# Optimization experiments

Hardware: AMD Instinct MI355X
Metric: run time of the kernel (lower is better)

The kernel has to match this reference:

```python
import jax, jax.numpy as jnp
import numpy as np

N = 50000
E = 600000
D = 128
HEADS = 4
G = 64  # num graphs
EPS = 1e-5


def setup_inputs() -> dict:
    key = jax.random.key(0)
    ks = jax.random.split(key, 16)
    s = 0.05
    inp = {
        'x': jax.random.normal(ks[0], (N, D), jnp.float32),
        'edge_index': jax.random.randint(ks[1], (2, E), 0, N, jnp.int64),
        'batch': jnp.sort(jax.random.randint(ks[2], (N,), 0, G, jnp.int64)),
        # GCN layer 1
        'W1': jax.random.normal(ks[3], (D, D), jnp.float32) * s,
        'b1': jnp.zeros((D,), jnp.float32),
        'g1': jnp.ones((D,), jnp.float32),
        'beta1': jnp.zeros((D,), jnp.float32),
        # GCN layer 2
        'W2': jax.random.normal(ks[4], (D, D), jnp.float32) * s,
        'b2': jnp.zeros((D,), jnp.float32),
        'g2': jnp.ones((D,), jnp.float32),
        'beta2': jnp.zeros((D,), jnp.float32),
        # GAT (heads=4, concat=False -> mean over heads)
        'gat_W': jax.random.normal(ks[5], (D, HEADS * D), jnp.float32) * s,
        'att_src': jax.random.normal(ks[6], (HEADS, D), jnp.float32) * s,
        'att_dst': jax.random.normal(ks[7], (HEADS, D), jnp.float32) * s,
        'gat_b': jnp.zeros((D,), jnp.float32),
    }
    return inp


def _layer_norm(x, g, b):
    mu = jnp.mean(x, axis=-1, keepdims=True)
    var = jnp.mean((x - mu) ** 2, axis=-1, keepdims=True)
    return (x - mu) * jax.lax.rsqrt(var + EPS) * g + b


def _gcn(x, W, b, src, dst, deg_inv_sqrt):
    h = x @ W                                    # [N, D]
    norm = deg_inv_sqrt[src] * deg_inv_sqrt[dst]  # [E']
    msg = norm[:, None] * h[src]                 # [E', D] gather
    return jax.ops.segment_sum(msg, dst, num_segments=N) + b


def _gat(x, W, b, att_src, att_dst, src, dst):
    h = (x @ W).reshape(N, HEADS, D)             # [N, H, D]
    a_s = jnp.einsum('nhd,hd->nh', h, att_src)   # [N, H]
    a_d = jnp.einsum('nhd,hd->nh', h, att_dst)
    e = jax.nn.leaky_relu(a_s[src] + a_d[dst], 0.2)          # [E', H]
    m = jax.ops.segment_max(e, dst, num_segments=N)          # segment softmax
    ex = jnp.exp(e - m[dst])
    den = jax.ops.segment_sum(ex, dst, num_segments=N)
    alpha = ex / den[dst]                                     # [E', H]
    out = jax.ops.segment_sum(alpha[:, :, None] * h[src], dst, num_segments=N)
    return jnp.mean(out, axis=1) + b             # concat=False -> head mean


def reference(x, edge_index, batch, W1, b1, g1, beta1, W2, b2, g2, beta2,
              gat_W, gat_b, att_src, att_dst):
    # add self loops (PyG default for GCNConv and GATConv)
    loops = jnp.arange(N, dtype=edge_index.dtype)
    src = jnp.concatenate([edge_index[0], loops])
    dst = jnp.concatenate([edge_index[1], loops])
    deg = jax.ops.segment_sum(jnp.ones_like(dst, jnp.float32), dst, num_segments=N)
    deg_inv_sqrt = jnp.where(deg > 0, jax.lax.rsqrt(jnp.maximum(deg, 1.0)), 0.0)

    # GCN stack: conv -> LayerNorm -> relu -> dropout(eval=identity)
    h = jax.nn.relu(_layer_norm(_gcn(x, W1, b1, src, dst, deg_inv_sqrt), g1, beta1))
    h = jax.nn.relu(_layer_norm(_gcn(h, W2, b2, src, dst, deg_inv_sqrt), g2, beta2))

    h = jax.nn.relu(_gat(h, gat_W, gat_b, att_src, att_dst, src, dst))
    node_embeddings = h

    cnt = jax.ops.segment_sum(jnp.ones((N,), jnp.float32), batch, num_segments=G)
    mean_pool = jax.ops.segment_sum(h, batch, num_segments=G) / jnp.maximum(cnt, 1.0)[:, None]
    max_pool = jax.ops.segment_max(h, batch, num_segments=G)
    graph_embedding = jnp.concatenate([mean_pool, max_pool], axis=1)  # [G, 2D]
    return graph_embedding, node_embeddings
```

## Files before the change

### kernel.cpp

```cpp
#include <hip/hip_runtime.h>
#include <math.h>


#define TPB 256

typedef __attribute__((ext_vector_type(8))) short short8;
typedef __attribute__((ext_vector_type(4))) float f32x4;
union U4S8 { uint4 u; short8 s; };

__device__ __forceinline__ float lrelu(float x) { return x > 0.f ? x : 0.2f * x; }

__device__ __forceinline__ unsigned short f2bf(float f) {
    unsigned int u = __float_as_uint(f);
    u += 0x7fffu + ((u >> 16) & 1u);
    return (unsigned short)(u >> 16);
}
__device__ __forceinline__ float2 bf2x(unsigned int u) {
    return make_float2(__uint_as_float(u << 16), __uint_as_float(u & 0xffff0000u));
}
__device__ __forceinline__ float sel4(float4 v, int h) {
    float r = v.x;
    r = (h == 1) ? v.y : r;
    r = (h == 2) ? v.z : r;
    r = (h == 3) ? v.w : r;
    return r;
}
__device__ __forceinline__ float dot4(f32x4 a, float4 b) {
    return a.x * b.x + a.y * b.y + a.z * b.z + a.w * b.w;
}

__global__ __launch_bounds__(TPB) void k_hist(const int* __restrict__ dst,
                                              int* __restrict__ deg, int e) {
    int i = blockIdx.x * TPB + threadIdx.x;
    if (i < e) atomicAdd(&deg[dst[i]], 1);
}

__global__ __launch_bounds__(TPB) void k_scan_part_wt(const int* __restrict__ deg,
                                                      int* __restrict__ part, int n, int nb,
                                                      const float* __restrict__ W1,
                                                      const float* __restrict__ W2,
                                                      const float* __restrict__ Wg,
                                                      unsigned short* __restrict__ Wt1,
                                                      unsigned short* __restrict__ Wt2,
                                                      unsigned short* __restrict__ Wtg) {
    int bid = blockIdx.x;
    if (bid < nb) {
        int i = bid * TPB + threadIdx.x;
        int v = (i < n) ? deg[i] : 0;
#pragma unroll
        for (int o = 32; o > 0; o >>= 1) v += __shfl_xor(v, o);
        __shared__ int sw[4];
        if ((threadIdx.x & 63) == 0) sw[threadIdx.x >> 6] = v;
        __syncthreads();
        if (threadIdx.x == 0) part[bid] = sw[0] + sw[1] + sw[2] + sw[3];
    } else {
        int i = (bid - nb) * TPB + threadIdx.x;
        if (i < 16384) {
            int k = i >> 7, c = i & 127;
            Wt1[c * 128 + k] = f2bf(W1[i]);
        } else if (i < 32768) {
            int j = i - 16384;
            int k = j >> 7, c = j & 127;
            Wt2[c * 128 + k] = f2bf(W2[j]);
        } else if (i < 98304) {
            int j = i - 32768;
            int k = j >> 9, c = j & 511;
            Wtg[c * 128 + k] = f2bf(Wg[j]);
        }
    }
}

__global__ __launch_bounds__(TPB) void k_scan_apply(const int* __restrict__ deg,
                                                    const int* __restrict__ part,
                                                    int* __restrict__ row_start,
                                                    int* __restrict__ cursor,
                                                    float* __restrict__ dis,
                                                    int n, int e_total) {
    __shared__ int sm[TPB];
    __shared__ int sred[4];
    int t = threadIdx.x;
    int bid = blockIdx.x;
    int pv = (t < bid) ? part[t] : 0;
#pragma unroll
    for (int o = 32; o > 0; o >>= 1) pv += __shfl_xor(pv, o);
    if ((t & 63) == 0) sred[t >> 6] = pv;
    __syncthreads();
    int basep = sred[0] + sred[1] + sred[2] + sred[3];
    int i = bid * TPB + t;
    int d = (i < n) ? deg[i] : 0;
    sm[t] = d;
    __syncthreads();
    for (int off = 1; off < TPB; off <<= 1) {
        int u = (t >= off) ? sm[t - off] : 0;
        __syncthreads();
        sm[t] += u;
        __syncthreads();
    }
    if (i < n) {
        int rs = basep + sm[t] - d;
        row_start[i] = rs;
        cursor[i] = rs;
        dis[i] = rsqrtf((float)(d + 1));
    }
    if (bid == 0 && t == 0) row_start[n] = e_total;
}

__global__ __launch_bounds__(TPB, 2) void k_gemm1_scatter(const float* __restrict__ feat,
                                                          const unsigned short* __restrict__ Wt,
                                                          unsigned short* __restrict__ C,
                                                          int nrows, int gb,
                                                          const int* __restrict__ src,
                                                          const int* __restrict__ dst,
                                                          const float* __restrict__ dis,
                                                          int* __restrict__ cursor,
                                                          int* __restrict__ csr_src,
                                                          float* __restrict__ csr_w, int e) {
    __shared__ uint4 wl[2048];
    int t = threadIdx.x;
    if (blockIdx.x >= gb) {
        int i = (blockIdx.x - gb) * TPB + t;
        if (i < e) {
            int s = src[i];
            int p = atomicAdd(&cursor[dst[i]], 1);
            csr_src[p] = s;
            csr_w[p] = dis[s];
        }
        return;
    }
#pragma unroll
    for (int i = 0; i < 8; ++i) {
        int fi = i * 256 + t;
        int l = fi & 63, ct = (fi >> 6) & 7, ks = fi >> 9;
        int chan = ct * 16 + (l & 15);
        wl[fi] = ((const uint4*)(Wt + (size_t)chan * 128))[ks * 4 + (l >> 4)];
    }
    __syncthreads();

    int wave = t >> 6, lane = t & 63;
    int wr = wave >> 1, wc = wave & 1;
    int nbase = (blockIdx.x << 7) + (wc << 6);
    const float4* brow[4];
#pragma unroll
    for (int nt = 0; nt < 4; ++nt) {
        int node = nbase + nt * 16 + (lane & 15);
        node = node < nrows ? node : (nrows - 1);
        brow[nt] = (const float4*)(feat + (size_t)node * 128);
    }
    f32x4 acc[4][4];
#pragma unroll
    for (int mt = 0; mt < 4; ++mt)
#pragma unroll
        for (int nt = 0; nt < 4; ++nt) acc[mt][nt] = (f32x4)0.f;

    int kq = lane >> 4;
#pragma unroll
    for (int ks = 0; ks < 4; ++ks) {
        U4S8 a[4], b[4];
#pragma unroll
        for (int mt = 0; mt < 4; ++mt)
            a[mt].u = wl[(ks * 8 + wr * 4 + mt) * 64 + lane];
#pragma unroll
        for (int nt = 0; nt < 4; ++nt) {
            float4 f0 = brow[nt][ks * 8 + kq * 2];
            float4 f1 = brow[nt][ks * 8 + kq * 2 + 1];
            b[nt].u.x = (unsigned int)f2bf(f0.x) | ((unsigned int)f2bf(f0.y) << 16);
            b[nt].u.y = (unsigned int)f2bf(f0.z) | ((unsigned int)f2bf(f0.w) << 16);
            b[nt].u.z = (unsigned int)f2bf(f1.x) | ((unsigned int)f2bf(f1.y) << 16);
            b[nt].u.w = (unsigned int)f2bf(f1.z) | ((unsigned int)f2bf(f1.w) << 16);
        }
#pragma unroll
        for (int mt = 0; mt < 4; ++mt)
#pragma unroll
            for (int nt = 0; nt < 4; ++nt)
                acc[mt][nt] = __builtin_amdgcn_mfma_f32_16x16x32_bf16(
                    a[mt].s, b[nt].s, acc[mt][nt], 0, 0, 0);
    }
#pragma unroll
    for (int nt = 0; nt < 4; ++nt) {
        int node = nbase + nt * 16 + (lane & 15);
        if (node >= nrows) continue;
#pragma unroll
        for (int mt = 0; mt < 4; ++mt) {
            int chan = (wr << 6) + mt * 16 + (lane >> 4) * 4;
            f32x4 v = acc[mt][nt];
            unsigned int p0 = (unsigned int)f2bf(v.x) | ((unsigned int)f2bf(v.y) << 16);
            unsigned int p1 = (unsigned int)f2bf(v.z) | ((unsigned int)f2bf(v.w) << 16);
            *(uint2*)(C + (size_t)node * 128 + chan) = make_uint2(p0, p1);
        }
    }
}

__global__ __launch_bounds__(TPB, 2) void k_gemm_mfma(const unsigned short* __restrict__ feat,
                                                      const unsigned short* __restrict__ Wt,
                                                      unsigned short* __restrict__ C,
                                                      int nrows, int ocols,
                                                      const float* __restrict__ att_s,
                                                      const float* __restrict__ att_d,
                                                      float* __restrict__ a_s,
                                                      float* __restrict__ a_d) {
    __shared__ uint4 wl[2048];
    __shared__ float sas[128], sad[128];
    int t = threadIdx.x;
    int cb = blockIdx.y << 7;
#pragma unroll
    for (int i = 0; i < 8; ++i) {
        int fi = i * 256 + t;
        int l = fi & 63, ct = (fi >> 6) & 7, ks = fi >> 9;
        int chan = cb + ct * 16 + (l & 15);
        wl[fi] = ((const uint4*)(Wt + (size_t)chan * 128))[ks * 4 + (l >> 4)];
    }
    __syncthreads();

    int wave = t >> 6, lane = t & 63;
    int wr = wave >> 1, wc = wave & 1;
    int nbase = (blockIdx.x << 7) + (wc << 6);
    const uint4* brow[4];
#pragma unroll
    for (int nt = 0; nt < 4; ++nt) {
        int node = nbase + nt * 16 + (lane & 15);
        node = node < nrows ? node : (nrows - 1);
        brow[nt] = (const uint4*)(feat + (size_t)node * 128);
    }
    f32x4 acc[4][4];
#pragma unroll
    for (int mt = 0; mt < 4; ++mt)
#pragma unroll
        for (int nt = 0; nt < 4; ++nt) acc[mt][nt] = (f32x4)0.f;

    int kq = lane >> 4;
#pragma unroll
    for (int ks = 0; ks < 4; ++ks) {
        U4S8 a[4], b[4];
#pragma unroll
        for (int mt = 0; mt < 4; ++mt)
            a[mt].u = wl[(ks * 8 + wr * 4 + mt) * 64 + lane];
#pragma unroll
        for (int nt = 0; nt < 4; ++nt)
            b[nt].u = brow[nt][ks * 4 + kq];
#pragma unroll
        for (int mt = 0; mt < 4; ++mt)
#pragma unroll
            for (int nt = 0; nt < 4; ++nt)
                acc[mt][nt] = __builtin_amdgcn_mfma_f32_16x16x32_bf16(
                    a[mt].s, b[nt].s, acc[mt][nt], 0, 0, 0);
    }
#pragma unroll
    for (int nt = 0; nt < 4; ++nt) {
        int node = nbase + nt * 16 + (lane & 15);
        if (node >= nrows) continue;
#pragma unroll
        for (int mt = 0; mt < 4; ++mt) {
            int chan = cb + (wr << 6) + mt * 16 + (lane >> 4) * 4;
            f32x4 v = acc[mt][nt];
            unsigned int p0 = (unsigned int)f2bf(v.x) | ((unsigned int)f2bf(v.y) << 16);
            unsigned int p1 = (unsigned int)f2bf(v.z) | ((unsigned int)f2bf(v.w) << 16);
            *(uint2*)(C + (size_t)node * ocols + chan) = make_uint2(p0, p1);
        }
    }
    if (att_s) {
        if (t < 128) { sas[t] = 0.f; sad[t] = 0.f; }
        __syncthreads();
        int h = blockIdx.y;
        float4 asv[4], adv[4];
#pragma unroll
        for (int mt = 0; mt < 4; ++mt) {
            int cbase = h * 128 + (wr << 6) + mt * 16 + (lane >> 4) * 4;
            asv[mt] = *(const float4*)(att_s + cbase);
            adv[mt] = *(const float4*)(att_d + cbase);
        }
#pragma unroll
        for (int nt = 0; nt < 4; ++nt) {
            float ds = 0.f, dd = 0.f;
#pragma unroll
            for (int mt = 0; mt < 4; ++mt) {
                ds += dot4(acc[mt][nt], asv[mt]);
                dd += dot4(acc[mt][nt], adv[mt]);
            }
            ds += __shfl_xor(ds, 16); ds += __shfl_xor(ds, 32);
            dd += __shfl_xor(dd, 16); dd += __shfl_xor(dd, 32);
            if (lane < 16) {
                atomicAdd(&sas[(wc << 6) + nt * 16 + lane], ds);
                atomicAdd(&sad[(wc << 6) + nt * 16 + lane], dd);
            }
        }
        __syncthreads();
        if (t < 128) {
            int node = (blockIdx.x << 7) + t;
            if (node < nrows) a_s[node * 4 + h] = sas[t];
        } else {
            int t2 = t - 128;
            int node = (blockIdx.x << 7) + t2;
            if (node < nrows) a_d[node * 4 + h] = sad[t2];
        }
    }
}

__global__ __launch_bounds__(TPB) void k_gcn_fused(const unsigned short* __restrict__ hb,
                                                   const int* __restrict__ csr_src,
                                                   const float* __restrict__ csr_w,
                                                   const int* __restrict__ row_start,
                                                   const float* __restrict__ dis,
                                                   const float* __restrict__ b,
                                                   const float* __restrict__ g,
                                                   const float* __restrict__ beta,
                                                   unsigned short* __restrict__ out, int n) {
    int node = (blockIdx.x * TPB + threadIdx.x) >> 6;
    int lane = threadIdx.x & 63;
    if (node >= n) return;
    int s0 = row_start[node], s1 = row_start[node + 1];
    float dn = dis[node];
    const uint4* hq = (const uint4*)hb;
    int q = lane >> 4, fl = lane & 15;
    float acc[8];
#pragma unroll
    for (int i = 0; i < 8; ++i) acc[i] = 0.f;
    for (int base = s0; base < s1; base += 64) {
        int cnt = min(64, s1 - base);
        int sidx = 0; float w = 0.f;
        if (lane < cnt) {
            sidx = csr_src[base + lane];
            w = csr_w[base + lane];
        }
        for (int j = 0; j < cnt; j += 16) {
            int j0 = j + q, j1 = j + 4 + q, j2 = j + 8 + q, j3 = j + 12 + q;
            int   sA = __shfl(sidx, j0), sB = __shfl(sidx, j1);
            int   sC = __shfl(sidx, j2), sD = __shfl(sidx, j3);
            float wA = __shfl(w, j0), wB = __shfl(w, j1);
            float wC = __shfl(w, j2), wD = __shfl(w, j3);
            uint4 uA = hq[(size_t)sA * 16 + fl];
            uint4 uB = hq[(size_t)sB * 16 + fl];
            uint4 uC = hq[(size_t)sC * 16 + fl];
            uint4 uD = hq[(size_t)sD * 16 + fl];
            float2 p0 = bf2x(uA.x), p1 = bf2x(uA.y), p2 = bf2x(uA.z), p3 = bf2x(uA.w);
            acc[0] += wA * p0.x; acc[1] += wA * p0.y;
            acc[2] += wA * p1.x; acc[3] += wA * p1.y;
            acc[4] += wA * p2.x; acc[5] += wA * p2.y;
            acc[6] += wA * p3.x; acc[7] += wA * p3.y;
            p0 = bf2x(uB.x); p1 = bf2x(uB.y); p2 = bf2x(uB.z); p3 = bf2x(uB.w);
            acc[0] += wB * p0.x; acc[1] += wB * p0.y;
            acc[2] += wB * p1.x; acc[3] += wB * p1.y;
            acc[4] += wB * p2.x; acc[5] += wB * p2.y;
            acc[6] += wB * p3.x; acc[7] += wB * p3.y;
            p0 = bf2x(uC.x); p1 = bf2x(uC.y); p2 = bf2x(uC.z); p3 = bf2x(uC.w);
            acc[0] += wC * p0.x; acc[1] += wC * p0.y;
            acc[2] += wC * p1.x; acc[3] += wC * p1.y;
            acc[4] += wC * p2.x; acc[5] += wC * p2.y;
            acc[6] += wC * p3.x; acc[7] += wC * p3.y;
            p0 = bf2x(uD.x); p1 = bf2x(uD.y); p2 = bf2x(uD.z); p3 = bf2x(uD.w);
            acc[0] += wD * p0.x; acc[1] += wD * p0.y;
            acc[2] += wD * p1.x; acc[3] += wD * p1.y;
            acc[4] += wD * p2.x; acc[5] += wD * p2.y;
            acc[6] += wD * p3.x; acc[7] += wD * p3.y;
        }
    }
#pragma unroll
    for (int i = 0; i < 8; ++i) {
        acc[i] += __shfl_xor(acc[i], 16);
        acc[i] += __shfl_xor(acc[i], 32);
    }
    float sl = dn * dn;
    uint4 us = hq[(size_t)node * 16 + fl];
    float2 h0 = bf2x(us.x), h1 = bf2x(us.y), h2 = bf2x(us.z), h3 = bf2x(us.w);
    float4 b0 = ((const float4*)b)[fl * 2], b1 = ((const float4*)b)[fl * 2 + 1];
    float v[8];
    v[0] = dn * acc[0] + sl * h0.x + b0.x;
    v[1] = dn * acc[1] + sl * h0.y + b0.y;
    v[2] = dn * acc[2] + sl * h1.x + b0.z;
    v[3] = dn * acc[3] + sl * h1.y + b0.w;
    v[4] = dn * acc[4] + sl * h2.x + b1.x;
    v[5] = dn * acc[5] + sl * h2.y + b1.y;
    v[6] = dn * acc[6] + sl * h3.x + b1.z;
    v[7] = dn * acc[7] + sl * h3.y + b1.w;
    float s = 0.f, sq = 0.f;
#pragma unroll
    for (int i = 0; i < 8; ++i) { s += v[i]; sq += v[i] * v[i]; }
#pragma unroll
    for (int o = 8; o > 0; o >>= 1) {
        s  += __shfl_xor(s, o);
        sq += __shfl_xor(sq, o);
    }
    float mu = s * (1.f / 128.f);
    float var = sq * (1.f / 128.f) - mu * mu;
    float rstd = rsqrtf(var + 1e-5f);
    float4 g0  = ((const float4*)g)[fl * 2],    g1v = ((const float4*)g)[fl * 2 + 1];
    float4 bt0 = ((const float4*)beta)[fl * 2], bt1 = ((const float4*)beta)[fl * 2 + 1];
    float o0 = fmaxf((v[0] - mu) * rstd * g0.x + bt0.x, 0.f);
    float o1 = fmaxf((v[1] - mu) * rstd * g0.y + bt0.y, 0.f);
    float o2 = fmaxf((v[2] - mu) * rstd * g0.z + bt0.z, 0.f);
    float o3 = fmaxf((v[3] - mu) * rstd * g0.w + bt0.w, 0.f);
    float o4 = fmaxf((v[4] - mu) * rstd * g1v.x + bt1.x, 0.f);
    float o5 = fmaxf((v[5] - mu) * rstd * g1v.y + bt1.y, 0.f);
    float o6 = fmaxf((v[6] - mu) * rstd * g1v.z + bt1.z, 0.f);
    float o7 = fmaxf((v[7] - mu) * rstd * g1v.w + bt1.w, 0.f);
    if (q == 0) {
        uint4 pk;
        pk.x = (unsigned int)f2bf(o0) | ((unsigned int)f2bf(o1) << 16);
        pk.y = (unsigned int)f2bf(o2) | ((unsigned int)f2bf(o3) << 16);
        pk.z = (unsigned int)f2bf(o4) | ((unsigned int)f2bf(o5) << 16);
        pk.w = (unsigned int)f2bf(o6) | ((unsigned int)f2bf(o7) << 16);
        ((uint4*)out)[(size_t)node * 16 + fl] = pk;
    }
}

__global__ __launch_bounds__(TPB) void k_gat_fused(const unsigned short* __restrict__ hgb,
                                                   const float* __restrict__ a_s,
                                                   const float* __restrict__ a_d,
                                                   const int* __restrict__ csr_src,
                                                   const int* __restrict__ row_start,
                                                   const float* __restrict__ gat_b,
                                                   float* __restrict__ node_out, int n) {
    __shared__ int   ssrc[4][64];
    __shared__ float swt[4][4][65];
    int node = (blockIdx.x * TPB + threadIdx.x) >> 6;
    int lane = threadIdx.x & 63;
    int wid = threadIdx.x >> 6;
    if (node >= n) return;
    int s0 = row_start[node], s1 = row_start[node + 1];
    int h = lane >> 4;
    const float4* as4 = (const float4*)a_s;
    float4 ad = ((const float4*)a_d)[node];
    float4 asn = as4[node];
    float4 wself;
    wself.x = __expf(lrelu(asn.x + ad.x));
    wself.y = __expf(lrelu(asn.y + ad.y));
    wself.z = __expf(lrelu(asn.z + ad.z));
    wself.w = __expf(lrelu(asn.w + ad.w));
    const uint4* hq = (const uint4*)hgb;
    float acc[8];
    {
        float wsh = sel4(wself, h);
        uint4 u = hq[(size_t)node * 64 + lane];
        float2 p0 = bf2x(u.x), p1 = bf2x(u.y), p2 = bf2x(u.z), p3 = bf2x(u.w);
        acc[0] = wsh * p0.x; acc[1] = wsh * p0.y;
        acc[2] = wsh * p1.x; acc[3] = wsh * p1.y;
        acc[4] = wsh * p2.x; acc[5] = wsh * p2.y;
        acc[6] = wsh * p3.x; acc[7] = wsh * p3.y;
    }
    float4 den = make_float4(0.f, 0.f, 0.f, 0.f);
    for (int base = s0; base < s1; base += 64) {
        int cnt = min(64, s1 - base);
        int sidx = 0;
        float4 w4 = make_float4(0.f, 0.f, 0.f, 0.f);
        if (lane < cnt) {
            sidx = csr_src[base + lane];
            float4 a = as4[sidx];
            w4.x = __expf(lrelu(a.x + ad.x));
            w4.y = __expf(lrelu(a.y + ad.y));
            w4.z = __expf(lrelu(a.z + ad.z));
            w4.w = __expf(lrelu(a.w + ad.w));
            den.x += w4.x; den.y += w4.y; den.z += w4.z; den.w += w4.w;
        }
        ssrc[wid][lane] = sidx;
        swt[wid][0][lane] = w4.x;
        swt[wid][1][lane] = w4.y;
        swt[wid][2][lane] = w4.z;
        swt[wid][3][lane] = w4.w;
        int j = 0;
        for (; j + 4 <= cnt; j += 4) {
            int sa = ssrc[wid][j + 0], sb = ssrc[wid][j + 1];
            int sc = ssrc[wid][j + 2], sd = ssrc[wid][j + 3];
            float wa = swt[wid][h][j + 0], wb = swt[wid][h][j + 1];
            float wc = swt[wid][h][j + 2], wd = swt[wid][h][j + 3];
            uint4 ua = hq[(size_t)sa * 64 + lane];
            uint4 ub = hq[(size_t)sb * 64 + lane];
            uint4 uc = hq[(size_t)sc * 64 + lane];
            uint4 ud = hq[(size_t)sd * 64 + lane];
            float2 p0, p1, p2, p3;
            p0 = bf2x(ua.x); p1 = bf2x(ua.y); p2 = bf2x(ua.z); p3 = bf2x(ua.w);
            acc[0] += wa * p0.x; acc[1] += wa * p0.y; acc[2] += wa * p1.x; acc[3] += wa * p1.y;
            acc[4] += wa * p2.x; acc[5] += wa * p2.y; acc[6] += wa * p3.x; acc[7] += wa * p3.y;
            p0 = bf2x(ub.x); p1 = bf2x(ub.y); p2 = bf2x(ub.z); p3 = bf2x(ub.w);
            acc[0] += wb * p0.x; acc[1] += wb * p0.y; acc[2] += wb * p1.x; acc[3] += wb * p1.y;
            acc[4] += wb * p2.x; acc[5] += wb * p2.y; acc[6] += wb * p3.x; acc[7] += wb * p3.y;
            p0 = bf2x(uc.x); p1 = bf2x(uc.y); p2 = bf2x(uc.z); p3 = bf2x(uc.w);
            acc[0] += wc * p0.x; acc[1] += wc * p0.y; acc[2] += wc * p1.x; acc[3] += wc * p1.y;
            acc[4] += wc * p2.x; acc[5] += wc * p2.y; acc[6] += wc * p3.x; acc[7] += wc * p3.y;
            p0 = bf2x(ud.x); p1 = bf2x(ud.y); p2 = bf2x(ud.z); p3 = bf2x(ud.w);
            acc[0] += wd * p0.x; acc[1] += wd * p0.y; acc[2] += wd * p1.x; acc[3] += wd * p1.y;
            acc[4] += wd * p2.x; acc[5] += wd * p2.y; acc[6] += wd * p3.x; acc[7] += wd * p3.y;
        }
        for (; j < cnt; ++j) {
            int s = ssrc[wid][j];
            float wj = swt[wid][h][j];
            uint4 u = hq[(size_t)s * 64 + lane];
            float2 p0 = bf2x(u.x), p1 = bf2x(u.y), p2 = bf2x(u.z), p3 = bf2x(u.w);
            acc[0] += wj * p0.x; acc[1] += wj * p0.y;
            acc[2] += wj * p1.x; acc[3] += wj * p1.y;
            acc[4] += wj * p2.x; acc[5] += wj * p2.y;
            acc[6] += wj * p3.x; acc[7] += wj * p3.y;
        }
    }
#pragma unroll
    for (int o = 32; o > 0; o >>= 1) {
        den.x += __shfl_xor(den.x, o);
        den.y += __shfl_xor(den.y, o);
        den.z += __shfl_xor(den.z, o);
        den.w += __shfl_xor(den.w, o);
    }
    den.x += wself.x; den.y += wself.y; den.z += wself.z; den.w += wself.w;
    float winv = 0.25f / sel4(den, h);
#pragma unroll
    for (int j = 0; j < 8; ++j) acc[j] *= winv;
#pragma unroll
    for (int j = 0; j < 8; ++j) acc[j] += __shfl_xor(acc[j], 16);
#pragma unroll
    for (int j = 0; j < 8; ++j) acc[j] += __shfl_xor(acc[j], 32);
    int fl = lane & 15;
    float4 gb0 = ((const float4*)gat_b)[fl * 2], gb1 = ((const float4*)gat_b)[fl * 2 + 1];
    if (lane < 16) {
        float4* o4 = (float4*)(node_out + (size_t)node * 128 + fl * 8);
        o4[0] = make_float4(fmaxf(acc[0] + gb0.x, 0.f), fmaxf(acc[1] + gb0.y, 0.f),
                            fmaxf(acc[2] + gb0.z, 0.f), fmaxf(acc[3] + gb0.w, 0.f));
        o4[1] = make_float4(fmaxf(acc[4] + gb1.x, 0.f), fmaxf(acc[5] + gb1.y, 0.f),
                            fmaxf(acc[6] + gb1.z, 0.f), fmaxf(acc[7] + gb1.w, 0.f));
    }
}

__global__ __launch_bounds__(TPB) void k_pool(const float* __restrict__ node_out,
                                              const int* __restrict__ batch,
                                              float* __restrict__ mean_acc,
                                              float* __restrict__ max_acc,
                                              float* __restrict__ cnt, int n) {
    int wave = (blockIdx.x * TPB + threadIdx.x) >> 6;
    int lane = threadIdx.x & 63;
    int n0 = wave * 16;
    if (n0 >= n) return;
    int n1 = min(n0 + 16, n);
    float2 bsum = make_float2(0.f, 0.f), bmax = make_float2(0.f, 0.f);
    int cur_g = batch[n0];
    int cntloc = 0;
    for (int nn = n0; nn < n1; ++nn) {
        int g = batch[nn];
        if (g != cur_g) {
            float* ma = mean_acc + cur_g * 128 + lane * 2;
            atomicAdd(ma + 0, bsum.x);
            atomicAdd(ma + 1, bsum.y);
            int* mxp = (int*)(max_acc + cur_g * 128 + lane * 2);
            atomicMax(mxp + 0, __float_as_int(bmax.x));
            atomicMax(mxp + 1, __float_as_int(bmax.y));
            if (lane == 0) atomicAdd(&cnt[cur_g], (float)cntloc);
            bsum = make_float2(0.f, 0.f);
            bmax = make_float2(0.f, 0.f);
            cntloc = 0;
            cur_g = g;
        }
        float2 o = ((const float2*)node_out)[(size_t)nn * 64 + lane];
        bsum.x += o.x; bsum.y += o.y;
        bmax.x = fmaxf(bmax.x, o.x); bmax.y = fmaxf(bmax.y, o.y);
        ++cntloc;
    }
    float* ma = mean_acc + cur_g * 128 + lane * 2;
    atomicAdd(ma + 0, bsum.x);
    atomicAdd(ma + 1, bsum.y);
    int* mxp = (int*)(max_acc + cur_g * 128 + lane * 2);
    atomicMax(mxp + 0, __float_as_int(bmax.x));
    atomicMax(mxp + 1, __float_as_int(bmax.y));
    if (lane == 0) atomicAdd(&cnt[cur_g], (float)cntloc);
}

__global__ __launch_bounds__(TPB) void k_pool_final(const float* __restrict__ mean_acc,
                                                    const float* __restrict__ max_acc,
                                                    const float* __restrict__ cnt,
                                                    float* __restrict__ gout, int g128) {
    int i = blockIdx.x * TPB + threadIdx.x;
    if (i >= g128) return;
    int g = i >> 7, d = i & 127;
    float c = fmaxf(cnt[g], 1.f);
    gout[g * 256 + d] = mean_acc[i] / c;
    gout[g * 256 + 128 + d] = max_acc[i];
}

extern "C" void kernel_launch(void* const* d_in, const int* in_sizes, int n_in,
                              void* d_out, int out_size, void* d_ws, size_t ws_size,
                              hipStream_t stream) {
    const float* x       = (const float*)d_in[0];
    const int*   ei      = (const int*)d_in[1];
    const int*   batch   = (const int*)d_in[2];
    const float* W1      = (const float*)d_in[3];
    const float* b1      = (const float*)d_in[4];
    const float* g1      = (const float*)d_in[5];
    const float* beta1   = (const float*)d_in[6];
    const float* W2      = (const float*)d_in[7];
    const float* b2      = (const float*)d_in[8];
    const float* g2      = (const float*)d_in[9];
    const float* beta2   = (const float*)d_in[10];
    const float* gat_W   = (const float*)d_in[11];
    const float* att_src = (const float*)d_in[12];
    const float* att_dst = (const float*)d_in[13];
    const float* gat_b   = (const float*)d_in[14];

    const int N = in_sizes[0] / 128;
    const int E = in_sizes[1] / 2;
    const int G = (out_size - N * 128) / 256;
    const int* src = ei;
    const int* dst = ei + E;

    float* ws = (float*)d_ws;
    float* dis      = ws; ws += N;
    float* a_s      = ws; ws += N * 4;
    float* a_d      = ws; ws += N * 4;
    float* mean_acc = ws; ws += G * 128;
    float* max_acc  = ws; ws += G * 128;
    float* cnt      = ws; ws += G;
    int* deg        = (int*)ws; ws += N;
    float* csr_w    = ws; ws += E;
    unsigned short* Hbf = (unsigned short*)ws; ws += (size_t)N * 64;
    unsigned short* Bbf = (unsigned short*)ws; ws += (size_t)N * 64;
    unsigned short* Cbf = (unsigned short*)ws; ws += (size_t)N * 64;
    unsigned short* hgb = (unsigned short*)ws; ws += (size_t)N * 256;
    unsigned short* Wt1 = (unsigned short*)ws; ws += 128 * 64;
    unsigned short* Wt2 = (unsigned short*)ws; ws += 128 * 64;
    unsigned short* Wtg = (unsigned short*)ws; ws += 512 * 64;
    int* part      = (int*)ws; ws += 256;
    int* row_start = (int*)ws; ws += N + 1;
    int* cursor    = (int*)ws; ws += N + 1;
    int* csr_src   = (int*)ws; ws += E;

    float* gout = (float*)d_out;
    float* node_out = gout + G * 256;

    auto cdiv = [](long a, long b) { return (int)((a + b - 1) / b); };
    const int nb = cdiv(N, TPB);

    hipMemsetAsync(mean_acc, 0, (size_t)(G * 256 + G + N) * 4, stream);
    k_hist<<<cdiv(E, TPB), TPB, 0, stream>>>(dst, deg, E);
    k_scan_part_wt<<<nb + cdiv(98304, TPB), TPB, 0, stream>>>(deg, part, N, nb,
                                                              W1, W2, gat_W, Wt1, Wt2, Wtg);
    k_scan_apply<<<nb, TPB, 0, stream>>>(deg, part, row_start, cursor, dis, N, E);

    const int gb = cdiv(N, 128);
    k_gemm1_scatter<<<gb + cdiv(E, TPB), TPB, 0, stream>>>(x, Wt1, Hbf, N, gb,
                                                           src, dst, dis, cursor,
                                                           csr_src, csr_w, E);
    k_gcn_fused<<<cdiv((long)N * 64, TPB), TPB, 0, stream>>>(Hbf, csr_src, csr_w, row_start, dis,
                                                             b1, g1, beta1, Bbf, N);
    k_gemm_mfma<<<dim3(cdiv(N, 128), 1), TPB, 0, stream>>>(Bbf, Wt2, Hbf, N, 128,
                                                           nullptr, nullptr, nullptr, nullptr);
    k_gcn_fused<<<cdiv((long)N * 64, TPB), TPB, 0, stream>>>(Hbf, csr_src, csr_w, row_start, dis,
                                                             b2, g2, beta2, Cbf, N);
    k_gemm_mfma<<<dim3(cdiv(N, 128), 4), TPB, 0, stream>>>(Cbf, Wtg, hgb, N, 512,
                                                           att_src, att_dst, a_s, a_d);
    k_gat_fused<<<cdiv((long)N * 64, TPB), TPB, 0, stream>>>(hgb, a_s, a_d, csr_src, row_start,
                                                             gat_b, node_out, N);

    k_pool<<<cdiv((long)cdiv(N, 16) * 64, TPB), TPB, 0, stream>>>(node_out, batch,
                                                                  mean_acc, max_acc, cnt, N);
    k_pool_final<<<cdiv((long)G * 128, TPB), TPB, 0, stream>>>(mean_acc, max_acc, cnt, gout, G * 128);
}
```

Baseline: 407.2 us.

## Quantize GAT projected features to int8 with per-node-head scales

The GAT projection GEMM now stores its output as int8 with a per-node, per-head absmax scale instead of bf16. The scale is packed next to the source attention logit and folded into the edge weights in the aggregation kernel. This halves the bytes gathered per edge in the memory-bound GAT aggregation and the GEMM write traffic. The cost is extra quantization error relative to bf16 features and one more float4 load per edge.

Result: faster. 376.1 us (-7.6%).

```diff
diff --git a/kernel.cpp b/kernel.cpp
--- a/kernel.cpp
+++ b/kernel.cpp
@@ -27,6 +27,16 @@
 }
 __device__ __forceinline__ float dot4(f32x4 a, float4 b) {
     return a.x * b.x + a.y * b.y + a.z * b.z + a.w * b.w;
+}
+__device__ __forceinline__ void unp8(uint2 u, float* f) {
+    f[0] = (float)(int)(char)(u.x & 0xff);
+    f[1] = (float)(int)(char)((u.x >> 8) & 0xff);
+    f[2] = (float)(int)(char)((u.x >> 16) & 0xff);
+    f[3] = (float)(int)(char)(u.x >> 24);
+    f[4] = (float)(int)(char)(u.y & 0xff);
+    f[5] = (float)(int)(char)((u.y >> 8) & 0xff);
+    f[6] = (float)(int)(char)((u.y >> 16) & 0xff);
+    f[7] = (float)(int)(char)(u.y >> 24);
 }
 
 __global__ __launch_bounds__(TPB) void k_hist(const int* __restrict__ dst,
@@ -196,10 +206,11 @@
                                                       int nrows, int ocols,
                                                       const float* __restrict__ att_s,
                                                       const float* __restrict__ att_d,
-                                                      float* __restrict__ a_s,
-                                                      float* __restrict__ a_d) {
+                                                      float* __restrict__ asn_sc,
+                                                      float* __restrict__ a_d,
+                                                      unsigned char* __restrict__ hgq) {
     __shared__ uint4 wl[2048];
-    __shared__ float sas[128], sad[128];
+    __shared__ float sas[128], sad[128], smax[128];
     int t = threadIdx.x;
     int cb = blockIdx.y << 7;
 #pragma unroll
@@ -244,53 +255,81 @@
                 acc[mt][nt] = __builtin_amdgcn_mfma_f32_16x16x32_bf16(
                     a[mt].s, b[nt].s, acc[mt][nt], 0, 0, 0);
     }
+    if (att_s == nullptr) {
+#pragma unroll
+        for (int nt = 0; nt < 4; ++nt) {
+            int node = nbase + nt * 16 + (lane & 15);
+            if (node >= nrows) continue;
+#pragma unroll
+            for (int mt = 0; mt < 4; ++mt) {
+                int chan = cb + (wr << 6) + mt * 16 + (lane >> 4) * 4;
+                f32x4 v = acc[mt][nt];
+                unsigned int p0 = (unsigned int)f2bf(v.x) | ((unsigned int)f2bf(v.y) << 16);
+                unsigned int p1 = (unsigned int)f2bf(v.z) | ((unsigned int)f2bf(v.w) << 16);
+                *(uint2*)(C + (size_t)node * ocols + chan) = make_uint2(p0, p1);
+            }
+        }
+        return;
+    }
+    if (t < 128) { sas[t] = 0.f; sad[t] = 0.f; smax[t] = 0.f; }
+    __syncthreads();
+    int h = blockIdx.y;
+    float4 asv[4], adv[4];
+#pragma unroll
+    for (int mt = 0; mt < 4; ++mt) {
+        int cbase = h * 128 + (wr << 6) + mt * 16 + (lane >> 4) * 4;
+        asv[mt] = *(const float4*)(att_s + cbase);
+        adv[mt] = *(const float4*)(att_d + cbase);
+    }
+#pragma unroll
+    for (int nt = 0; nt < 4; ++nt) {
+        float ds = 0.f, dd = 0.f, mx = 0.f;
+#pragma unroll
+        for (int mt = 0; mt < 4; ++mt) {
+            f32x4 v = acc[mt][nt];
+            ds += dot4(v, asv[mt]);
+            dd += dot4(v, adv[mt]);
+            mx = fmaxf(mx, fmaxf(fmaxf(fabsf(v.x), fabsf(v.y)),
+                                 fmaxf(fabsf(v.z), fabsf(v.w))));
+        }
+        ds += __shfl_xor(ds, 16); ds += __shfl_xor(ds, 32);
+        dd += __shfl_xor(dd, 16); dd += __shfl_xor(dd, 32);
+        mx = fmaxf(mx, __shfl_xor(mx, 16));
+        mx = fmaxf(mx, __shfl_xor(mx, 32));
+        if (lane < 16) {
+            int sl = (wc << 6) + nt * 16 + lane;
+            atomicAdd(&sas[sl], ds);
+            atomicAdd(&sad[sl], dd);
+            atomicMax((int*)&smax[sl], __float_as_int(mx));
+        }
+    }
+    __syncthreads();
+    if (t < 128) {
+        int node = (blockIdx.x << 7) + t;
+        if (node < nrows) {
+            asn_sc[(size_t)node * 8 + h] = sas[t];
+            asn_sc[(size_t)node * 8 + 4 + h] = smax[t] * (1.f / 127.f);
+        }
+    } else {
+        int t2 = t - 128;
+        int node = (blockIdx.x << 7) + t2;
+        if (node < nrows) a_d[(size_t)node * 4 + h] = sad[t2];
+    }
 #pragma unroll
     for (int nt = 0; nt < 4; ++nt) {
         int node = nbase + nt * 16 + (lane & 15);
         if (node >= nrows) continue;
+        float mxv = smax[(wc << 6) + nt * 16 + (lane & 15)];
+        float rs = mxv > 0.f ? 127.f / mxv : 0.f;
 #pragma unroll
         for (int mt = 0; mt < 4; ++mt) {
-            int chan = cb + (wr << 6) + mt * 16 + (lane >> 4) * 4;
+            int chan = (wr << 6) + mt * 16 + (lane >> 4) * 4;
             f32x4 v = acc[mt][nt];
-            unsigned int p0 = (unsigned int)f2bf(v.x) | ((unsigned int)f2bf(v.y) << 16);
-            unsigned int p1 = (unsigned int)f2bf(v.z) | ((unsigned int)f2bf(v.w) << 16);
-            *(uint2*)(C + (size_t)node * ocols + chan) = make_uint2(p0, p1);
-        }
-    }
-    if (att_s) {
-        if (t < 128) { sas[t] = 0.f; sad[t] = 0.f; }
-        __syncthreads();
-        int h = blockIdx.y;
-        float4 asv[4], adv[4];
-#pragma unroll
-        for (int mt = 0; mt < 4; ++mt) {
-            int cbase = h * 128 + (wr << 6) + mt * 16 + (lane >> 4) * 4;
-            asv[mt] = *(const float4*)(att_s + cbase);
-            adv[mt] = *(const float4*)(att_d + cbase);
-        }
-#pragma unroll
-        for (int nt = 0; nt < 4; ++nt) {
-            float ds = 0.f, dd = 0.f;
-#pragma unroll
-            for (int mt = 0; mt < 4; ++mt) {
-                ds += dot4(acc[mt][nt], asv[mt]);
-                dd += dot4(acc[mt][nt], adv[mt]);
-            }
-            ds += __shfl_xor(ds, 16); ds += __shfl_xor(ds, 32);
-            dd += __shfl_xor(dd, 16); dd += __shfl_xor(dd, 32);
-            if (lane < 16) {
-                atomicAdd(&sas[(wc << 6) + nt * 16 + lane], ds);
-                atomicAdd(&sad[(wc << 6) + nt * 16 + lane], dd);
-            }
-        }
-        __syncthreads();
-        if (t < 128) {
-            int node = (blockIdx.x << 7) + t;
-            if (node < nrows) a_s[node * 4 + h] = sas[t];
-        } else {
-            int t2 = t - 128;
-            int node = (blockIdx.x << 7) + t2;
-            if (node < nrows) a_d[node * 4 + h] = sad[t2];
+            int q0 = (int)rintf(v.x * rs), q1 = (int)rintf(v.y * rs);
+            int q2 = (int)rintf(v.z * rs), q3 = (int)rintf(v.w * rs);
+            unsigned int pk = (q0 & 0xff) | ((q1 & 0xff) << 8) |
+                              ((q2 & 0xff) << 16) | ((unsigned int)(q3 & 0xff) << 24);
+            *(unsigned int*)(hgq + (size_t)node * 512 + h * 128 + chan) = pk;
         }
     }
 }
@@ -402,8 +441,8 @@
     }
 }
 
-__global__ __launch_bounds__(TPB) void k_gat_fused(const unsigned short* __restrict__ hgb,
-                                                   const float* __restrict__ a_s,
+__global__ __launch_bounds__(TPB) void k_gat_fused(const unsigned char* __restrict__ hgq,
+                                                   const float* __restrict__ asn_sc,
                                                    const float* __restrict__ a_d,
                                                    const int* __restrict__ csr_src,
                                                    const int* __restrict__ row_start,
@@ -416,25 +455,25 @@
     int wid = threadIdx.x >> 6;
     if (node >= n) return;
     int s0 = row_start[node], s1 = row_start[node + 1];
-    int h = lane >> 4;
-    const float4* as4 = (const float4*)a_s;
+    int h = lane >> 4, fl = lane & 15;
+    const float4* asc4 = (const float4*)asn_sc;
     float4 ad = ((const float4*)a_d)[node];
-    float4 asn = as4[node];
-    float4 wself;
-    wself.x = __expf(lrelu(asn.x + ad.x));
-    wself.y = __expf(lrelu(asn.y + ad.y));
-    wself.z = __expf(lrelu(asn.z + ad.z));
-    wself.w = __expf(lrelu(asn.w + ad.w));
-    const uint4* hq = (const uint4*)hgb;
+    float4 asn = asc4[node * 2];
+    float4 scn = asc4[node * 2 + 1];
+    float4 eself;
+    eself.x = __expf(lrelu(asn.x + ad.x));
+    eself.y = __expf(lrelu(asn.y + ad.y));
+    eself.z = __expf(lrelu(asn.z + ad.z));
+    eself.w = __expf(lrelu(asn.w + ad.w));
+    const uint2* hq2 = (const uint2*)hgq;
+    int hoff = (h << 4) + fl;
     float acc[8];
     {
-        float wsh = sel4(wself, h);
-        uint4 u = hq[(size_t)node * 64 + lane];
-        float2 p0 = bf2x(u.x), p1 = bf2x(u.y), p2 = bf2x(u.z), p3 = bf2x(u.w);
-        acc[0] = wsh * p0.x; acc[1] = wsh * p0.y;
-        acc[2] = wsh * p1.x; acc[3] = wsh * p1.y;
-        acc[4] = wsh * p2.x; acc[5] = wsh * p2.y;
-        acc[6] = wsh * p3.x; acc[7] = wsh * p3.y;
+        float wsh = sel4(eself, h) * sel4(scn, h);
+        float f[8];
+        unp8(hq2[(size_t)node * 64 + hoff], f);
+#pragma unroll
+        for (int i = 0; i < 8; ++i) acc[i] = wsh * f[i];
     }
     float4 den = make_float4(0.f, 0.f, 0.f, 0.f);
     for (int base = s0; base < s1; base += 64) {
@@ -443,12 +482,15 @@
         float4 w4 = make_float4(0.f, 0.f, 0.f, 0.f);
         if (lane < cnt) {
             sidx = csr_src[base + lane];
-            float4 a = as4[sidx];
-            w4.x = __expf(lrelu(a.x + ad.x));
-            w4.y = __expf(lrelu(a.y + ad.y));
-            w4.z = __expf(lrelu(a.z + ad.z));
-            w4.w = __expf(lrelu(a.w + ad.w));
-            den.x += w4.x; den.y += w4.y; den.z += w4.z; den.w += w4.w;
+            float4 a = asc4[sidx * 2];
+            float4 sc = asc4[sidx * 2 + 1];
+            float4 e4;
+            e4.x = __expf(lrelu(a.x + ad.x));
+            e4.y = __expf(lrelu(a.y + ad.y));
+            e4.z = __expf(lrelu(a.z + ad.z));
+            e4.w = __expf(lrelu(a.w + ad.w));
+            den.x += e4.x; den.y += e4.y; den.z += e4.z; den.w += e4.w;
+            w4 = make_float4(e4.x * sc.x, e4.y * sc.y, e4.z * sc.z, e4.w * sc.w);
         }
         ssrc[wid][lane] = sidx;
         swt[wid][0][lane] = w4.x;
@@ -461,33 +503,31 @@
             int sc = ssrc[wid][j + 2], sd = ssrc[wid][j + 3];
             float wa = swt[wid][h][j + 0], wb = swt[wid][h][j + 1];
             float wc = swt[wid][h][j + 2], wd = swt[wid][h][j + 3];
-            uint4 ua = hq[(size_t)sa * 64 + lane];
-            uint4 ub = hq[(size_t)sb * 64 + lane];
-            uint4 uc = hq[(size_t)sc * 64 + lane];
-            uint4 ud = hq[(size_t)sd * 64 + lane];
-            float2 p0, p1, p2, p3;
-            p0 = bf2x(ua.x); p1 = bf2x(ua.y); p2 = bf2x(ua.z); p3 = bf2x(ua.w);
-            acc[0] += wa * p0.x; acc[1] += wa * p0.y; acc[2] += wa * p1.x; acc[3] += wa * p1.y;
-            acc[4] += wa * p2.x; acc[5] += wa * p2.y; acc[6] += wa * p3.x; acc[7] += wa * p3.y;
-            p0 = bf2x(ub.x); p1 = bf2x(ub.y); p2 = bf2x(ub.z); p3 = bf2x(ub.w);
-            acc[0] += wb * p0.x; acc[1] += wb * p0.y; acc[2] += wb * p1.x; acc[3] += wb * p1.y;
-            acc[4] += wb * p2.x; acc[5] += wb * p2.y; acc[6] += wb * p3.x; acc[7] += wb * p3.y;
-            p0 = bf2x(uc.x); p1 = bf2x(uc.y); p2 = bf2x(uc.z); p3 = bf2x(uc.w);
-            acc[0] += wc * p0.x; acc[1] += wc * p0.y; acc[2] += wc * p1.x; acc[3] += wc * p1.y;
-            acc[4] += wc * p2.x; acc[5] += wc * p2.y; acc[6] += wc * p3.x; acc[7] += wc * p3.y;
-            p0 = bf2x(ud.x); p1 = bf2x(ud.y); p2 = bf2x(ud.z); p3 = bf2x(ud.w);
-            acc[0] += wd * p0.x; acc[1] += wd * p0.y; acc[2] += wd * p1.x; acc[3] += wd * p1.y;
-            acc[4] += wd * p2.x; acc[5] += wd * p2.y; acc[6] += wd * p3.x; acc[7] += wd * p3.y;
+            uint2 ua = hq2[(size_t)sa * 64 + hoff];
+            uint2 ub = hq2[(size_t)sb * 64 + hoff];
+            uint2 uc = hq2[(size_t)sc * 64 + hoff];
+            uint2 ud = hq2[(size_t)sd * 64 + hoff];
+            float f[8];
+            unp8(ua, f);
+#pragma unroll
+            for (int i = 0; i < 8; ++i) acc[i] += wa * f[i];
+            unp8(ub, f);
+#pragma unroll
+            for (int i = 0; i < 8; ++i) acc[i] += wb * f[i];
+            unp8(uc, f);
+#pragma unroll
+            for (int i = 0; i < 8; ++i) acc[i] += wc * f[i];
+            unp8(ud, f);
+#pragma unroll
+            for (int i = 0; i < 8; ++i) acc[i] += wd * f[i];
         }
         for (; j < cnt; ++j) {
             int s = ssrc[wid][j];
             float wj = swt[wid][h][j];
-            uint4 u = hq[(size_t)s * 64 + lane];
-            float2 p0 = bf2x(u.x), p1 = bf2x(u.y), p2 = bf2x(u.z), p3 = bf2x(u.w);
-            acc[0] += wj * p0.x; acc[1] += wj * p0.y;
-            acc[2] += wj * p1.x; acc[3] += wj * p1.y;
-            acc[4] += wj * p2.x; acc[5] += wj * p2.y;
-            acc[6] += wj * p3.x; acc[7] += wj * p3.y;
+            float f[8];
+            unp8(hq2[(size_t)s * 64 + hoff], f);
+#pragma unroll
+            for (int i = 0; i < 8; ++i) acc[i] += wj * f[i];
         }
     }
 #pragma unroll
@@ -497,7 +537,7 @@
         den.z += __shfl_xor(den.z, o);
         den.w += __shfl_xor(den.w, o);
     }
-    den.x += wself.x; den.y += wself.y; den.z += wself.z; den.w += wself.w;
+    den.x += eself.x; den.y += eself.y; den.z += eself.z; den.w += eself.w;
     float winv = 0.25f / sel4(den, h);
 #pragma unroll
     for (int j = 0; j < 8; ++j) acc[j] *= winv;
@@ -505,7 +545,6 @@
     for (int j = 0; j < 8; ++j) acc[j] += __shfl_xor(acc[j], 16);
 #pragma unroll
     for (int j = 0; j < 8; ++j) acc[j] += __shfl_xor(acc[j], 32);
-    int fl = lane & 15;
     float4 gb0 = ((const float4*)gat_b)[fl * 2], gb1 = ((const float4*)gat_b)[fl * 2 + 1];
     if (lane < 16) {
         float4* o4 = (float4*)(node_out + (size_t)node * 128 + fl * 8);
@@ -597,7 +636,7 @@
 
     float* ws = (float*)d_ws;
     float* dis      = ws; ws += N;
-    float* a_s      = ws; ws += N * 4;
+    float* asn_sc   = ws; ws += (size_t)N * 8;
     float* a_d      = ws; ws += N * 4;
     float* mean_acc = ws; ws += G * 128;
     float* max_acc  = ws; ws += G * 128;
@@ -607,7 +646,7 @@
     unsigned short* Hbf = (unsigned short*)ws; ws += (size_t)N * 64;
     unsigned short* Bbf = (unsigned short*)ws; ws += (size_t)N * 64;
     unsigned short* Cbf = (unsigned short*)ws; ws += (size_t)N * 64;
-    unsigned short* hgb = (unsigned short*)ws; ws += (size_t)N * 256;
+    unsigned char* hgq  = (unsigned char*)ws; ws += (size_t)N * 128;
     unsigned short* Wt1 = (unsigned short*)ws; ws += 128 * 64;
     unsigned short* Wt2 = (unsigned short*)ws; ws += 128 * 64;
     unsigned short* Wtg = (unsigned short*)ws; ws += 512 * 64;
@@ -635,12 +674,12 @@
     k_gcn_fused<<<cdiv((long)N * 64, TPB), TPB, 0, stream>>>(Hbf, csr_src, csr_w, row_start, dis,
                                                              b1, g1, beta1, Bbf, N);
     k_gemm_mfma<<<dim3(cdiv(N, 128), 1), TPB, 0, stream>>>(Bbf, Wt2, Hbf, N, 128,
-                                                           nullptr, nullptr, nullptr, nullptr);
+                                                           nullptr, nullptr, nullptr, nullptr, nullptr);
     k_gcn_fused<<<cdiv((long)N * 64, TPB), TPB, 0, stream>>>(Hbf, csr_src, csr_w, row_start, dis,
                                                              b2, g2, beta2, Cbf, N);
-    k_gemm_mfma<<<dim3(cdiv(N, 128), 4), TPB, 0, stream>>>(Cbf, Wtg, hgb, N, 512,
-                                                           att_src, att_dst, a_s, a_d);
-    k_gat_fused<<<cdiv((long)N * 64, TPB), TPB, 0, stream>>>(hgb, a_s, a_d, csr_src, row_start,
+    k_gemm_mfma<<<dim3(cdiv(N, 128), 4), TPB, 0, stream>>>(Cbf, Wtg, nullptr, N, 512,
+                                                           att_src, att_dst, asn_sc, a_d, hgq);
+    k_gat_fused<<<cdiv((long)N * 64, TPB), TPB, 0, stream>>>(hgq, asn_sc, a_d, csr_src, row_start,
                                                              gat_b, node_out, N);
 
     k_pool<<<cdiv((long)cdiv(N, 16) * 64, TPB), TPB, 0, stream>>>(node_out, batch,
```
